# Kernel tuning notes

Hardware: AMD Instinct MI355X
Metric: run time of the kernel (lower is better)

Reference implementation:

```python
import jax, jax.numpy as jnp
import numpy as np

D_MODEL = 640
KW = 32                                  # kernel_width -> content_kernel (compression (1,1))
SUPER = np.array([5, 5, 2, 1, 1])        # supersampling per subhead
DIL = np.array([1, 1, 2, 4, 8])          # dilation rate per subhead
SUBHEADS = 5
HEADS = int(SUPER.sum())                 # 14
DH = D_MODEL // SUBHEADS                 # 128
B, N = 2, 1024
KC = KW                                  # content kernel width
DIL_PER_HEAD = np.repeat(DIL, SUPER)     # dilation used by each of the 14 value heads


def _windows(seq, bias, dil):
    """Banded (dilated, stride-1, 'same'-padded) windows of a projected sequence.

    seq: (B, N, DH). The original zero-pads the raw sequence, then applies the
    per-head Linear; projecting a zero vector yields the bias, so padding the
    projected sequence with `bias` is mathematically identical.
    Returns (B, N, KC, DH) with out[b, l, j] = padded[b, l + j*dil].
    """
    dil = int(dil)
    pad_total = (KC - 1) * dil           # effective kernel minus 1, stride 1 -> same length
    pl = pad_total // 2
    pr = pad_total - pl
    b = seq.shape[0]
    left = jnp.broadcast_to(bias, (b, pl, DH))
    right = jnp.broadcast_to(bias, (b, pr, DH))
    padded = jnp.concatenate([left, seq, right], axis=1)
    idx = jnp.arange(N)[:, None] + jnp.arange(KC)[None, :] * dil  # (N, KC)
    return padded[:, idx]


def setup_inputs() -> dict:
    key = jax.random.key(0)
    ks = jax.random.split(key, 13)
    f = lambda k, sh, s=1.0: jax.random.normal(k, sh, dtype=jnp.float32) * s
    return {
        "query": f(ks[0], (B, N, D_MODEL)),
        "key": f(ks[1], (B, N, D_MODEL)),
        "value": f(ks[2], (B, N, D_MODEL)),
        "Qk": f(ks[3], (SUBHEADS, DH, D_MODEL), 0.04),
        "Qb": f(ks[4], (SUBHEADS, DH), 0.02),
        "Kk": f(ks[5], (SUBHEADS, DH, D_MODEL), 0.04),
        "Kb": f(ks[6], (SUBHEADS, DH), 0.02),
        "Vk": f(ks[7], (HEADS, DH, D_MODEL), 0.04),
        "Vb": f(ks[8], (HEADS, DH), 0.02),
        "Sk": f(ks[9], (HEADS, KC, KC), 0.1),   # Pos_Sampling kernel, Kq=1 so in=out=KC
        "Sb": f(ks[10], (HEADS, KC), 0.02),
        "Ck": f(ks[11], (D_MODEL, HEADS * DH), 0.02),  # Collapse kernel
        "Cb": f(ks[12], (D_MODEL,), 0.0),
    }


def reference(query, key, value, Qk, Qb, Kk, Kb, Vk, Vb, Sk, Sb, Ck, Cb):
    # Per-subhead Q/K projections (query_kernel=1, stride=1 -> one query per position)
    q = jnp.einsum('bnd,sod->bnso', query, Qk) + Qb          # (B,N,5,DH)
    kproj = jnp.einsum('bnd,sod->bnso', key, Kk) + Kb        # (B,N,5,DH)
    kwin = jnp.stack(
        [_windows(kproj[:, :, s], Kb[s], DIL[s]) for s in range(SUBHEADS)],
        axis=2)                                              # (B,N,5,KC,DH)
    # Banded scores (original applies no 1/sqrt(d) scaling)
    score = jnp.einsum('bnsd,bnskd->bnsk', q, kwin)          # (B,N,5,KC)
    # Supersample subhead scores into heads, then learned positional resampling
    score = jnp.repeat(score, SUPER, axis=2, total_repeat_length=HEADS)  # (B,N,14,KC)
    score = jnp.einsum('bnhk,hjk->bnhj', score, Sk) + Sb     # Pos_Sampling Linear
    w = jax.nn.softmax(score, axis=-1)
    # Per-head value projection; each head windows with its subhead's dilation
    vproj = jnp.einsum('bnd,hod->bnho', value, Vk) + Vb      # (B,N,14,DH)
    vwin = jnp.stack(
        [_windows(vproj[:, :, h], Vb[h], DIL_PER_HEAD[h]) for h in range(HEADS)],
        axis=2)                                              # (B,N,14,KC,DH)
    attn = jnp.einsum('bnhk,bnhkd->bnhd', w, vwin)           # (B,N,14,DH)
    flat = attn.reshape(attn.shape[0], attn.shape[1], HEADS * DH)
    return jnp.einsum('bnf,of->bno', flat, Ck) + Cb          # (B,N,D_MODEL)
```

## Files before the change

kernel.cpp:

```cpp
#include <hip/hip_runtime.h>
#include <hip/hip_bf16.h>

using bf16 = __hip_bfloat16;
typedef __attribute__((ext_vector_type(8))) short s16x8;
typedef __attribute__((ext_vector_type(4))) float f32x4;
typedef unsigned int u32;

__device__ __forceinline__ float b2f(short u) {
    union { float f; u32 i; } x; x.i = ((u32)(unsigned short)u) << 16; return x.f;
}
__device__ __forceinline__ short f2b(float f) {
    bf16 h = (bf16)f; return *(short*)&h;
}

__device__ __forceinline__ void glds16(const bf16* g, bf16* l) {
#if __has_builtin(__builtin_amdgcn_global_load_lds)
    __builtin_amdgcn_global_load_lds(
        (const __attribute__((address_space(1))) u32*)g,
        (__attribute__((address_space(3))) u32*)l, 16, 0, 0);
#else
    *(uint4*)l = *(const uint4*)g;
#endif
}

struct CvtArgs { const float* src[10]; bf16* dst[10]; int n[10]; int bb[11]; };
__global__ __launch_bounds__(256)
void convert_kernel(CvtArgs a) {
    const int blk = blockIdx.x;
    int s = 0;
    while (s < 9 && blk >= a.bb[s + 1]) ++s;
    const int base = (blk - a.bb[s]) * 1024 + threadIdx.x * 4;
    if (base >= a.n[s]) return;
    float4 v = *(const float4*)(a.src[s] + base);
    ushort4 o;
    o.x = (unsigned short)f2b(v.x); o.y = (unsigned short)f2b(v.y);
    o.z = (unsigned short)f2b(v.z); o.w = (unsigned short)f2b(v.w);
    *(ushort4*)(a.dst[s] + base) = o;
}

template<bool A_F32, bool OUT_F32>
__device__ __forceinline__ void gemm64(
    const void* __restrict__ A, const bf16* __restrict__ W,
    const bf16* __restrict__ bias, void* __restrict__ out,
    int m0, int n0, int N, int K, bf16* lA, bf16* lB) {
    const int tid = threadIdx.x;
    const int wave = tid >> 6, lane = tid & 63;
    const int wr = wave >> 1, wc = wave & 1;
    const int quad = lane >> 4, lm = lane & 15;
    const int srow = tid >> 2, scol8 = (tid & 3) * 8;
    f32x4 acc[2][2] = {};
    for (int k0 = 0; k0 < K; k0 += 32) {
        if (A_F32) {
            const float* g = (const float*)A + (size_t)(m0 + srow) * K + k0 + scol8;
            float4 f0 = *(const float4*)g;
            float4 f1 = *(const float4*)(g + 4);
            union { uint4 u; short h[8]; } p;
            p.h[0] = f2b(f0.x); p.h[1] = f2b(f0.y); p.h[2] = f2b(f0.z); p.h[3] = f2b(f0.w);
            p.h[4] = f2b(f1.x); p.h[5] = f2b(f1.y); p.h[6] = f2b(f1.z); p.h[7] = f2b(f1.w);
            *(uint4*)(lA + tid * 8) = p.u;
        } else {
            glds16((const bf16*)A + (size_t)(m0 + srow) * K + k0 + scol8, lA + tid * 8);
        }
        glds16(W + (size_t)(n0 + srow) * K + k0 + scol8, lB + tid * 8);
        __syncthreads();
        s16x8 af[2], bf[2];
#pragma unroll
        for (int i = 0; i < 2; ++i)
            af[i] = *(const s16x8*)&lA[(wr * 32 + i * 16 + lm) * 32 + quad * 8];
#pragma unroll
        for (int j = 0; j < 2; ++j)
            bf[j] = *(const s16x8*)&lB[(wc * 32 + j * 16 + lm) * 32 + quad * 8];
#pragma unroll
        for (int i = 0; i < 2; ++i)
#pragma unroll
            for (int j = 0; j < 2; ++j)
                acc[i][j] = __builtin_amdgcn_mfma_f32_16x16x32_bf16(af[i], bf[j], acc[i][j], 0, 0, 0);
        __syncthreads();
    }
#pragma unroll
    for (int i = 0; i < 2; ++i) {
        const int rbase = m0 + wr * 32 + i * 16 + quad * 4;
#pragma unroll
        for (int j = 0; j < 2; ++j) {
            const int col = n0 + wc * 32 + j * 16 + lm;
            const float bv = (float)bias[col];
#pragma unroll
            for (int r = 0; r < 4; ++r) {
                float v = acc[i][j][r] + bv;
                size_t off = (size_t)(rbase + r) * N + col;
                if (OUT_F32) ((float*)out)[off] = v;
                else         ((bf16*)out)[off] = (bf16)v;
            }
        }
    }
}

__global__ __launch_bounds__(256)
void proj_kernel(const float* __restrict__ q, const float* __restrict__ k,
                 const float* __restrict__ v,
                 const bf16* __restrict__ Qkc, const bf16* __restrict__ Kkc,
                 const bf16* __restrict__ Vkc,
                 const bf16* __restrict__ Qbc, const bf16* __restrict__ Kbc,
                 const bf16* __restrict__ Vbc,
                 float* __restrict__ qp, float* __restrict__ kp,
                 bf16* __restrict__ vp) {
    __shared__ __align__(16) bf16 lA[64 * 32];
    __shared__ __align__(16) bf16 lB[64 * 32];
    const int L = blockIdx.x, xcd = L & 7, i = L >> 3;
    const int m0 = (xcd * 4 + i / 48) * 64;
    const int nid = i % 48;
    if (nid < 10)
        gemm64<true, true >(q, Qkc, Qbc, qp, m0, nid * 64, 640, 640, lA, lB);
    else if (nid < 20)
        gemm64<true, true >(k, Kkc, Kbc, kp, m0, (nid - 10) * 64, 640, 640, lA, lB);
    else
        gemm64<true, false>(v, Vkc, Vbc, vp, m0, (nid - 20) * 64, 1792, 640, lA, lB);
}

__global__ __launch_bounds__(256)
void collapse_kernel(const bf16* __restrict__ atn, const bf16* __restrict__ Ckc,
                     const bf16* __restrict__ Cbc, float* __restrict__ out) {
    __shared__ __align__(16) bf16 lA[64 * 32];
    __shared__ __align__(16) bf16 lB[64 * 32];
    const int L = blockIdx.x, xcd = L & 7, i = L >> 3;
    const int m0 = (xcd * 4 + i / 10) * 64;
    const int n0 = (i % 10) * 64;
    gemm64<false, true>(atn, Ckc, Cbc, out, m0, n0, 640, 1792, lA, lB);
}

__global__ __launch_bounds__(256)
void attn_v3(const float* __restrict__ qp, const float* __restrict__ kp,
             const bf16* __restrict__ vp,
             const bf16* __restrict__ Kbc, const bf16* __restrict__ Vbc,
             const bf16* __restrict__ Skc, const bf16* __restrict__ Sbc,
             bf16* __restrict__ atn) {
    const int pos = ((blockIdx.x & 7) << 8) | (blockIdx.x >> 3);
    const int b = pos >> 10, l = pos & 1023;
    const int t = threadIdx.x;
    __shared__ float qs[640];
    __shared__ float partA[5 * 256];
    __shared__ float sc5[5 * 32];
    __shared__ float sc14[14 * 32];
    __shared__ float w14[14 * 32];

    for (int i = t; i < 640; i += 256) qs[i] = qp[(size_t)pos * 640 + i];
    __syncthreads();

    {
        const int j = t >> 3, cbase = (t & 7) * 16;
#pragma unroll
        for (int s = 0; s < 5; ++s) {
            const int dil = (s < 2) ? 1 : (1 << (s - 1));
            const int pl = (31 * dil) >> 1;
            const int row = l + j * dil - pl;
            const float* q = qs + s * 128 + cbase;
            float acc = 0.f;
            if (row >= 0 && row < 1024) {
                const float* kr = kp + (size_t)((b << 10) | row) * 640 + s * 128 + cbase;
#pragma unroll
                for (int c = 0; c < 16; c += 4) {
                    float4 kv = *(const float4*)(kr + c);
                    acc += q[c] * kv.x + q[c + 1] * kv.y + q[c + 2] * kv.z + q[c + 3] * kv.w;
                }
            } else {
                const bf16* kb = Kbc + s * 128 + cbase;
#pragma unroll
                for (int c = 0; c < 16; ++c) acc += q[c] * (float)kb[c];
            }
            partA[s * 256 + t] = acc;
        }
    }
    __syncthreads();
    if (t < 160) {
        const int s = t >> 5, j = t & 31;
        const float* p = partA + s * 256 + j * 8;
        sc5[s * 32 + j] = ((p[0] + p[1]) + (p[2] + p[3])) + ((p[4] + p[5]) + (p[6] + p[7]));
    }
    __syncthreads();

    for (int idx = t; idx < 448; idx += 256) {
        const int h = idx >> 5;
        const int s = (h < 5) ? 0 : (h < 10) ? 1 : (h < 12) ? 2 : (h == 12) ? 3 : 4;
        const s16x8* sk = (const s16x8*)((const short*)Skc + idx * 32);
        const float* sc = sc5 + s * 32;
        float acc = b2f(((const short*)Sbc)[idx]);
#pragma unroll
        for (int g = 0; g < 4; ++g) {
            s16x8 kk = sk[g];
#pragma unroll
            for (int r = 0; r < 8; ++r) acc += sc[g * 8 + r] * b2f(kk[r]);
        }
        sc14[idx] = acc;
    }
    __syncthreads();

    if (t < 14) {
        const float* srow = sc14 + t * 32;
        float* wrow = w14 + t * 32;
        float mx = srow[0];
        for (int j = 1; j < 32; ++j) mx = fmaxf(mx, srow[j]);
        float sum = 0.f;
        for (int j = 0; j < 32; ++j) { float e = __expf(srow[j] - mx); wrow[j] = e; sum += e; }
        float inv = 1.f / sum;
        for (int j = 0; j < 32; ++j) wrow[j] *= inv;
    }
    __syncthreads();

    if (t < 224) {
        const int h = t >> 4, d8 = (t & 15) * 8;
        const int dil = (h < 10) ? 1 : (h < 12) ? 2 : (h == 12) ? 4 : 8;
        const int pl = (31 * dil) >> 1;
        const int col = h * 128 + d8;
        const float* wrow = w14 + h * 32;
        float acc[8] = {};
#pragma unroll
        for (int j = 0; j < 32; ++j) {
            const int row = l + j * dil - pl;
            const short* src = (row >= 0 && row < 1024)
                ? (const short*)vp + (size_t)((b << 10) | row) * 1792 + col
                : (const short*)Vbc + col;
            s16x8 v8 = *(const s16x8*)src;
            const float w = wrow[j];
#pragma unroll
            for (int r = 0; r < 8; ++r) acc[r] += w * b2f(v8[r]);
        }
        union { uint4 u; short h16[8]; } o;
#pragma unroll
        for (int r = 0; r < 8; ++r) o.h16[r] = f2b(acc[r]);
        *(uint4*)((short*)atn + (size_t)pos * 1792 + col) = o.u;
    }
}

extern "C" void kernel_launch(void* const* d_in, const int* in_sizes, int n_in,
                              void* d_out, int out_size, void* d_ws, size_t ws_size,
                              hipStream_t stream) {
    const int M = 2048;
    char* w = (char*)d_ws;
    size_t off = 0;
    auto alloc = [&](size_t bytes) -> char* {
        off = (off + 255) & ~(size_t)255;
        char* p = w + off; off += bytes; return p;
    };
    bf16* Qkc = (bf16*)alloc(409600 * 2);
    bf16* Qbc = (bf16*)alloc(640 * 2);
    bf16* Kkc = (bf16*)alloc(409600 * 2);
    bf16* Kbc = (bf16*)alloc(640 * 2);
    bf16* Vkc = (bf16*)alloc(1146880 * 2);
    bf16* Vbc = (bf16*)alloc(1792 * 2);
    bf16* Skc = (bf16*)alloc(14336 * 2);
    bf16* Sbc = (bf16*)alloc(448 * 2);
    bf16* Ckc = (bf16*)alloc(1146880 * 2);
    bf16* Cbc = (bf16*)alloc(640 * 2);
    float* qp = (float*)alloc((size_t)M * 640 * 4);
    float* kp = (float*)alloc((size_t)M * 640 * 4);
    bf16*  vp = (bf16*)alloc((size_t)M * 1792 * 2);
    bf16*  atn = (bf16*)alloc((size_t)M * 1792 * 2);

    CvtArgs ca;
    bf16* dsts[10] = {Qkc, Qbc, Kkc, Kbc, Vkc, Vbc, Skc, Sbc, Ckc, Cbc};
    const int ns[10] = {409600, 640, 409600, 640, 1146880, 1792, 14336, 448, 1146880, 640};
    int cum = 0;
    for (int i = 0; i < 10; ++i) {
        ca.src[i] = (const float*)d_in[3 + i];
        ca.dst[i] = dsts[i];
        ca.n[i] = ns[i];
        ca.bb[i] = cum;
        cum += (ns[i] + 1023) / 1024;
    }
    ca.bb[10] = cum;

    dim3 blk(256);
    convert_kernel<<<dim3(cum), blk, 0, stream>>>(ca);
    proj_kernel<<<dim3(32 * 48), blk, 0, stream>>>(
        (const float*)d_in[0], (const float*)d_in[1], (const float*)d_in[2],
        Qkc, Kkc, Vkc, Qbc, Kbc, Vbc, qp, kp, vp);
    attn_v3<<<dim3(2048), blk, 0, stream>>>(qp, kp, vp, Kbc, Vbc, Skc, Sbc, atn);
    collapse_kernel<<<dim3(320), blk, 0, stream>>>(atn, Ckc, Cbc, (float*)d_out);
}
```

Before: 183.1 us.

## Pre-convert activations to bf16, enlarge GEMM tiles, use shuffle reductions in attention

```diff
diff --git a/kernel.cpp b/kernel.cpp
--- a/kernel.cpp
+++ b/kernel.cpp
@@ -23,12 +23,12 @@
 #endif
 }
 
-struct CvtArgs { const float* src[10]; bf16* dst[10]; int n[10]; int bb[11]; };
+struct CvtArgs { const float* src[13]; bf16* dst[13]; int n[13]; int bb[14]; };
 __global__ __launch_bounds__(256)
 void convert_kernel(CvtArgs a) {
     const int blk = blockIdx.x;
     int s = 0;
-    while (s < 9 && blk >= a.bb[s + 1]) ++s;
+    while (s < 12 && blk >= a.bb[s + 1]) ++s;
     const int base = (blk - a.bb[s]) * 1024 + threadIdx.x * 4;
     if (base >= a.n[s]) return;
     float4 v = *(const float4*)(a.src[s] + base);
@@ -38,51 +38,50 @@
     *(ushort4*)(a.dst[s] + base) = o;
 }
 
-template<bool A_F32, bool OUT_F32>
-__device__ __forceinline__ void gemm64(
-    const void* __restrict__ A, const bf16* __restrict__ W,
+template<int BM, int BN, bool OUT_F32>
+__device__ __forceinline__ void gemm_core(
+    const bf16* __restrict__ A, const bf16* __restrict__ W,
     const bf16* __restrict__ bias, void* __restrict__ out,
     int m0, int n0, int N, int K, bf16* lA, bf16* lB) {
+    constexpr int WM = BM / 2, WN = BN / 2, FM = WM / 16, FN = WN / 16;
+    constexpr int SA = BM / 64, SB = BN / 64;
     const int tid = threadIdx.x;
     const int wave = tid >> 6, lane = tid & 63;
     const int wr = wave >> 1, wc = wave & 1;
     const int quad = lane >> 4, lm = lane & 15;
-    const int srow = tid >> 2, scol8 = (tid & 3) * 8;
-    f32x4 acc[2][2] = {};
+    f32x4 acc[FM][FN] = {};
     for (int k0 = 0; k0 < K; k0 += 32) {
-        if (A_F32) {
-            const float* g = (const float*)A + (size_t)(m0 + srow) * K + k0 + scol8;
-            float4 f0 = *(const float4*)g;
-            float4 f1 = *(const float4*)(g + 4);
-            union { uint4 u; short h[8]; } p;
-            p.h[0] = f2b(f0.x); p.h[1] = f2b(f0.y); p.h[2] = f2b(f0.z); p.h[3] = f2b(f0.w);
-            p.h[4] = f2b(f1.x); p.h[5] = f2b(f1.y); p.h[6] = f2b(f1.z); p.h[7] = f2b(f1.w);
-            *(uint4*)(lA + tid * 8) = p.u;
-        } else {
-            glds16((const bf16*)A + (size_t)(m0 + srow) * K + k0 + scol8, lA + tid * 8);
-        }
-        glds16(W + (size_t)(n0 + srow) * K + k0 + scol8, lB + tid * 8);
+#pragma unroll
+        for (int q = 0; q < SA; ++q) {
+            int sl = q * 256 + tid;
+            glds16(A + (size_t)(m0 + (sl >> 2)) * K + k0 + (sl & 3) * 8, lA + sl * 8);
+        }
+#pragma unroll
+        for (int q = 0; q < SB; ++q) {
+            int sl = q * 256 + tid;
+            glds16(W + (size_t)(n0 + (sl >> 2)) * K + k0 + (sl & 3) * 8, lB + sl * 8);
+        }
         __syncthreads();
-        s16x8 af[2], bf[2];
-#pragma unroll
-        for (int i = 0; i < 2; ++i)
-            af[i] = *(const s16x8*)&lA[(wr * 32 + i * 16 + lm) * 32 + quad * 8];
-#pragma unroll
-        for (int j = 0; j < 2; ++j)
-            bf[j] = *(const s16x8*)&lB[(wc * 32 + j * 16 + lm) * 32 + quad * 8];
-#pragma unroll
-        for (int i = 0; i < 2; ++i)
-#pragma unroll
-            for (int j = 0; j < 2; ++j)
-                acc[i][j] = __builtin_amdgcn_mfma_f32_16x16x32_bf16(af[i], bf[j], acc[i][j], 0, 0, 0);
+        s16x8 af[FM], bf_[FN];
+#pragma unroll
+        for (int i = 0; i < FM; ++i)
+            af[i] = *(const s16x8*)&lA[(wr * WM + i * 16 + lm) * 32 + quad * 8];
+#pragma unroll
+        for (int j = 0; j < FN; ++j)
+            bf_[j] = *(const s16x8*)&lB[(wc * WN + j * 16 + lm) * 32 + quad * 8];
+#pragma unroll
+        for (int i = 0; i < FM; ++i)
+#pragma unroll
+            for (int j = 0; j < FN; ++j)
+                acc[i][j] = __builtin_amdgcn_mfma_f32_16x16x32_bf16(af[i], bf_[j], acc[i][j], 0, 0, 0);
         __syncthreads();
     }
 #pragma unroll
-    for (int i = 0; i < 2; ++i) {
-        const int rbase = m0 + wr * 32 + i * 16 + quad * 4;
-#pragma unroll
-        for (int j = 0; j < 2; ++j) {
-            const int col = n0 + wc * 32 + j * 16 + lm;
+    for (int i = 0; i < FM; ++i) {
+        const int rbase = m0 + wr * WM + i * 16 + quad * 4;
+#pragma unroll
+        for (int j = 0; j < FN; ++j) {
+            const int col = n0 + wc * WN + j * 16 + lm;
             const float bv = (float)bias[col];
 #pragma unroll
             for (int r = 0; r < 4; ++r) {
@@ -96,40 +95,40 @@
 }
 
 __global__ __launch_bounds__(256)
-void proj_kernel(const float* __restrict__ q, const float* __restrict__ k,
-                 const float* __restrict__ v,
+void proj_kernel(const bf16* __restrict__ qc, const bf16* __restrict__ kc,
+                 const bf16* __restrict__ vc,
                  const bf16* __restrict__ Qkc, const bf16* __restrict__ Kkc,
                  const bf16* __restrict__ Vkc,
                  const bf16* __restrict__ Qbc, const bf16* __restrict__ Kbc,
                  const bf16* __restrict__ Vbc,
                  float* __restrict__ qp, float* __restrict__ kp,
                  bf16* __restrict__ vp) {
-    __shared__ __align__(16) bf16 lA[64 * 32];
+    __shared__ __align__(16) bf16 lA[128 * 32];
+    __shared__ __align__(16) bf16 lB[128 * 32];
+    const int L = blockIdx.x, xcd = L & 7, i = L >> 3;
+    const int m0 = (xcd * 2 + i / 24) * 128;
+    const int nid = i % 24;
+    if (nid < 5)
+        gemm_core<128, 128, true >(qc, Qkc, Qbc, qp, m0, nid * 128, 640, 640, lA, lB);
+    else if (nid < 10)
+        gemm_core<128, 128, true >(kc, Kkc, Kbc, kp, m0, (nid - 5) * 128, 640, 640, lA, lB);
+    else
+        gemm_core<128, 128, false>(vc, Vkc, Vbc, vp, m0, (nid - 10) * 128, 1792, 640, lA, lB);
+}
+
+__global__ __launch_bounds__(256)
+void collapse_kernel(const bf16* __restrict__ atn, const bf16* __restrict__ Ckc,
+                     const bf16* __restrict__ Cbc, float* __restrict__ out) {
+    __shared__ __align__(16) bf16 lA[128 * 32];
     __shared__ __align__(16) bf16 lB[64 * 32];
     const int L = blockIdx.x, xcd = L & 7, i = L >> 3;
-    const int m0 = (xcd * 4 + i / 48) * 64;
-    const int nid = i % 48;
-    if (nid < 10)
-        gemm64<true, true >(q, Qkc, Qbc, qp, m0, nid * 64, 640, 640, lA, lB);
-    else if (nid < 20)
-        gemm64<true, true >(k, Kkc, Kbc, kp, m0, (nid - 10) * 64, 640, 640, lA, lB);
-    else
-        gemm64<true, false>(v, Vkc, Vbc, vp, m0, (nid - 20) * 64, 1792, 640, lA, lB);
-}
-
-__global__ __launch_bounds__(256)
-void collapse_kernel(const bf16* __restrict__ atn, const bf16* __restrict__ Ckc,
-                     const bf16* __restrict__ Cbc, float* __restrict__ out) {
-    __shared__ __align__(16) bf16 lA[64 * 32];
-    __shared__ __align__(16) bf16 lB[64 * 32];
-    const int L = blockIdx.x, xcd = L & 7, i = L >> 3;
-    const int m0 = (xcd * 4 + i / 10) * 64;
+    const int m0 = (xcd * 2 + i / 10) * 128;
     const int n0 = (i % 10) * 64;
-    gemm64<false, true>(atn, Ckc, Cbc, out, m0, n0, 640, 1792, lA, lB);
-}
-
-__global__ __launch_bounds__(256)
-void attn_v3(const float* __restrict__ qp, const float* __restrict__ kp,
+    gemm_core<128, 64, true>(atn, Ckc, Cbc, out, m0, n0, 640, 1792, lA, lB);
+}
+
+__global__ __launch_bounds__(256)
+void attn_v4(const float* __restrict__ qp, const float* __restrict__ kp,
              const bf16* __restrict__ vp,
              const bf16* __restrict__ Kbc, const bf16* __restrict__ Vbc,
              const bf16* __restrict__ Skc, const bf16* __restrict__ Sbc,
@@ -138,43 +137,44 @@
     const int b = pos >> 10, l = pos & 1023;
     const int t = threadIdx.x;
     __shared__ float qs[640];
-    __shared__ float partA[5 * 256];
     __shared__ float sc5[5 * 32];
     __shared__ float sc14[14 * 32];
-    __shared__ float w14[14 * 32];
-
-    for (int i = t; i < 640; i += 256) qs[i] = qp[(size_t)pos * 640 + i];
+    __shared__ float w14T[32 * 14];
+
+    if (t < 160) ((float4*)qs)[t] = ((const float4*)(qp + (size_t)pos * 640))[t];
     __syncthreads();
 
     {
-        const int j = t >> 3, cbase = (t & 7) * 16;
+        const int j = t >> 3, p = t & 7;
 #pragma unroll
         for (int s = 0; s < 5; ++s) {
             const int dil = (s < 2) ? 1 : (1 << (s - 1));
             const int pl = (31 * dil) >> 1;
             const int row = l + j * dil - pl;
-            const float* q = qs + s * 128 + cbase;
+            const float* q = qs + s * 128 + p * 4;
             float acc = 0.f;
             if (row >= 0 && row < 1024) {
-                const float* kr = kp + (size_t)((b << 10) | row) * 640 + s * 128 + cbase;
-#pragma unroll
-                for (int c = 0; c < 16; c += 4) {
-                    float4 kv = *(const float4*)(kr + c);
-                    acc += q[c] * kv.x + q[c + 1] * kv.y + q[c + 2] * kv.z + q[c + 3] * kv.w;
+                const float* kr = kp + (size_t)((b << 10) | row) * 640 + s * 128 + p * 4;
+#pragma unroll
+                for (int g = 0; g < 4; ++g) {
+                    float4 kv = *(const float4*)(kr + g * 32);
+                    float4 qv = *(const float4*)(q + g * 32);
+                    acc += qv.x * kv.x + qv.y * kv.y + qv.z * kv.z + qv.w * kv.w;
                 }
             } else {
-                const bf16* kb = Kbc + s * 128 + cbase;
-#pragma unroll
-                for (int c = 0; c < 16; ++c) acc += q[c] * (float)kb[c];
+                const bf16* kb = Kbc + s * 128 + p * 4;
+#pragma unroll
+                for (int g = 0; g < 4; ++g) {
+                    float4 qv = *(const float4*)(q + g * 32);
+                    acc += qv.x * (float)kb[g * 32] + qv.y * (float)kb[g * 32 + 1]
+                         + qv.z * (float)kb[g * 32 + 2] + qv.w * (float)kb[g * 32 + 3];
+                }
             }
-            partA[s * 256 + t] = acc;
-        }
-    }
-    __syncthreads();
-    if (t < 160) {
-        const int s = t >> 5, j = t & 31;
-        const float* p = partA + s * 256 + j * 8;
-        sc5[s * 32 + j] = ((p[0] + p[1]) + (p[2] + p[3])) + ((p[4] + p[5]) + (p[6] + p[7]));
+            acc += __shfl_xor(acc, 1);
+            acc += __shfl_xor(acc, 2);
+            acc += __shfl_xor(acc, 4);
+            if (p == 0) sc5[s * 32 + j] = acc;
+        }
     }
     __syncthreads();
 
@@ -194,15 +194,19 @@
     }
     __syncthreads();
 
-    if (t < 14) {
-        const float* srow = sc14 + t * 32;
-        float* wrow = w14 + t * 32;
-        float mx = srow[0];
-        for (int j = 1; j < 32; ++j) mx = fmaxf(mx, srow[j]);
-        float sum = 0.f;
-        for (int j = 0; j < 32; ++j) { float e = __expf(srow[j] - mx); wrow[j] = e; sum += e; }
+    if (t < 224) {
+        const int h = t >> 4, u = t & 15;
+        float s0 = sc14[h * 32 + u], s1 = sc14[h * 32 + u + 16];
+        float mx = fmaxf(s0, s1);
+#pragma unroll
+        for (int m = 1; m < 16; m <<= 1) mx = fmaxf(mx, __shfl_xor(mx, m));
+        float e0 = __expf(s0 - mx), e1 = __expf(s1 - mx);
+        float sum = e0 + e1;
+#pragma unroll
+        for (int m = 1; m < 16; m <<= 1) sum += __shfl_xor(sum, m);
         float inv = 1.f / sum;
-        for (int j = 0; j < 32; ++j) wrow[j] *= inv;
+        w14T[u * 14 + h] = e0 * inv;
+        w14T[(u + 16) * 14 + h] = e1 * inv;
     }
     __syncthreads();
 
@@ -211,7 +215,6 @@
         const int dil = (h < 10) ? 1 : (h < 12) ? 2 : (h == 12) ? 4 : 8;
         const int pl = (31 * dil) >> 1;
         const int col = h * 128 + d8;
-        const float* wrow = w14 + h * 32;
         float acc[8] = {};
 #pragma unroll
         for (int j = 0; j < 32; ++j) {
@@ -220,7 +223,7 @@
                 ? (const short*)vp + (size_t)((b << 10) | row) * 1792 + col
                 : (const short*)Vbc + col;
             s16x8 v8 = *(const s16x8*)src;
-            const float w = wrow[j];
+            const float w = w14T[j * 14 + h];
 #pragma unroll
             for (int r = 0; r < 8; ++r) acc[r] += w * b2f(v8[r]);
         }
@@ -241,6 +244,9 @@
         off = (off + 255) & ~(size_t)255;
         char* p = w + off; off += bytes; return p;
     };
+    bf16* qc  = (bf16*)alloc(1310720 * 2);
+    bf16* kc  = (bf16*)alloc(1310720 * 2);
+    bf16* vc  = (bf16*)alloc(1310720 * 2);
     bf16* Qkc = (bf16*)alloc(409600 * 2);
     bf16* Qbc = (bf16*)alloc(640 * 2);
     bf16* Kkc = (bf16*)alloc(409600 * 2);
@@ -257,23 +263,23 @@
     bf16*  atn = (bf16*)alloc((size_t)M * 1792 * 2);
 
     CvtArgs ca;
-    bf16* dsts[10] = {Qkc, Qbc, Kkc, Kbc, Vkc, Vbc, Skc, Sbc, Ckc, Cbc};
-    const int ns[10] = {409600, 640, 409600, 640, 1146880, 1792, 14336, 448, 1146880, 640};
+    bf16* dsts[13] = {qc, kc, vc, Qkc, Qbc, Kkc, Kbc, Vkc, Vbc, Skc, Sbc, Ckc, Cbc};
+    const int ns[13] = {1310720, 1310720, 1310720, 409600, 640, 409600, 640,
+                        1146880, 1792, 14336, 448, 1146880, 640};
     int cum = 0;
-    for (int i = 0; i < 10; ++i) {
-        ca.src[i] = (const float*)d_in[3 + i];
+    for (int i = 0; i < 13; ++i) {
+        ca.src[i] = (const float*)d_in[i];
         ca.dst[i] = dsts[i];
         ca.n[i] = ns[i];
         ca.bb[i] = cum;
         cum += (ns[i] + 1023) / 1024;
     }
-    ca.bb[10] = cum;
+    ca.bb[13] = cum;
 
     dim3 blk(256);
     convert_kernel<<<dim3(cum), blk, 0, stream>>>(ca);
-    proj_kernel<<<dim3(32 * 48), blk, 0, stream>>>(
-        (const float*)d_in[0], (const float*)d_in[1], (const float*)d_in[2],
-        Qkc, Kkc, Vkc, Qbc, Kbc, Vbc, qp, kp, vp);
-    attn_v3<<<dim3(2048), blk, 0, stream>>>(qp, kp, vp, Kbc, Vbc, Skc, Sbc, atn);
-    collapse_kernel<<<dim3(320), blk, 0, stream>>>(atn, Ckc, Cbc, (float*)d_out);
-}
+    proj_kernel<<<dim3(384), blk, 0, stream>>>(qc, kc, vc, Qkc, Kkc, Vkc,
+                                               Qbc, Kbc, Vbc, qp, kp, vp);
+    attn_v4<<<dim3(2048), blk, 0, stream>>>(qp, kp, vp, Kbc, Vbc, Skc, Sbc, atn);
+    collapse_kernel<<<dim3(160), blk, 0, stream>>>(atn, Ckc, Cbc, (float*)d_out);
+}
```

After: 171.6 us. 1.07x faster.
